# Kernel optimization log

Hardware: AMD Instinct MI355X
Metric: run time of the kernel (lower is better)

## Reference

```python
import jax, jax.numpy as jnp
import numpy as np

N, C, A = 4096, 1000, 2048


def setup_inputs() -> dict:
    key = jax.random.key(0)
    k1, k2, k3, k4 = jax.random.split(key, 4)
    features = jax.random.normal(k1, (N, A), dtype=jnp.float32)
    labels = jax.random.randint(k2, (N,), 0, C, dtype=jnp.int64)
    cv_matrix = jax.random.uniform(k3, (N, A), dtype=jnp.float32)
    ratio = jnp.asarray(0.5, dtype=jnp.float32)
    weight = jax.random.normal(k4, (C, A), dtype=jnp.float32) * 0.02
    bias = jnp.zeros((C,), dtype=jnp.float32)
    return {"features": features, "labels": labels, "cv_matrix": cv_matrix,
            "ratio": ratio, "weight": weight, "bias": bias}


def reference(features, labels, cv_matrix, ratio, weight, bias):
    # logits = features @ W^T + b
    logits = features @ weight.T + bias  # [N, C]
    # sigma2[n,c] = ratio * sum_a (W[c,a] - W[y_n,a])^2 * cv[n,a]
    # Expand the square to avoid materializing the [N, C, A] tensor:
    #   = sum_a W[c,a]^2 cv - 2 sum_a W[c,a] (W[y,a] cv) + sum_a W[y,a]^2 cv
    Wy = weight[labels]                          # [N, A] gather of per-label rows
    t1 = cv_matrix @ (weight * weight).T         # [N, C]
    t2 = (cv_matrix * Wy) @ weight.T             # [N, C]
    t3 = jnp.sum(Wy * Wy * cv_matrix, axis=1, keepdims=True)  # [N, 1]
    sigma2 = ratio * (t1 - 2.0 * t2 + t3)        # [N, C]
    aug_logits = logits + 0.5 * sigma2
    # mean cross-entropy on augmented logits
    logp = jax.nn.log_softmax(aug_logits, axis=-1)
    nll = -jnp.take_along_axis(logp, labels[:, None], axis=1)[:, 0]
    loss = jnp.mean(nll)
    return loss, logits
```

## Files before the change

kernel.cpp:

```cpp
#include <hip/hip_runtime.h>
#include <hip/hip_bf16.h>

#define N_ROWS 4096
#define C_CLS  1000
#define C_PAD  1024
#define A_DIM  2048

typedef __attribute__((ext_vector_type(8))) short short8;
typedef __attribute__((ext_vector_type(4))) float f32x4;

__device__ __forceinline__ unsigned short f2bf(float x) {
    unsigned u = __float_as_uint(x);
    unsigned rounding = 0x7fffu + ((u >> 16) & 1u);
    return (unsigned short)((u + rounding) >> 16);
}

__device__ __forceinline__ unsigned pack2(float a, float b) {
    return (unsigned)f2bf(a) | ((unsigned)f2bf(b) << 16);
}

__device__ __forceinline__ void gload16(unsigned short* lds, const unsigned short* g) {
    __builtin_amdgcn_global_load_lds(
        (const __attribute__((address_space(1))) unsigned int*)g,
        (__attribute__((address_space(3))) unsigned int*)lds,
        16, 0, 0);
}

__global__ __launch_bounds__(256) void prep_all(
        const float* __restrict__ F, const float* __restrict__ CV,
        const float* __restrict__ W, const int* __restrict__ labels,
        const float* __restrict__ ratio_p,
        unsigned short* __restrict__ Fb, unsigned short* __restrict__ Ub,
        unsigned short* __restrict__ Vb,
        unsigned short* __restrict__ Wb, unsigned short* __restrict__ W2b,
        float* __restrict__ t3c) {
    int bid = blockIdx.x;
    if (bid >= N_ROWS) {
        int t = (bid - N_ROWS) * 256 + threadIdx.x;
        int a8 = t * 8;
        int c = a8 >> 11;
        int a = a8 & (A_DIM - 1);
        float4 w0 = make_float4(0.f, 0.f, 0.f, 0.f);
        float4 w1 = make_float4(0.f, 0.f, 0.f, 0.f);
        if (c < C_CLS) {
            w0 = *(const float4*)(W + (size_t)c * A_DIM + a);
            w1 = *(const float4*)(W + (size_t)c * A_DIM + a + 4);
        }
        uint4 pw, pw2;
        pw.x  = pack2(w0.x, w0.y);  pw.y  = pack2(w0.z, w0.w);
        pw.z  = pack2(w1.x, w1.y);  pw.w  = pack2(w1.z, w1.w);
        pw2.x = pack2(w0.x*w0.x, w0.y*w0.y);  pw2.y = pack2(w0.z*w0.z, w0.w*w0.w);
        pw2.z = pack2(w1.x*w1.x, w1.y*w1.y);  pw2.w = pack2(w1.z*w1.z, w1.w*w1.w);
        *(uint4*)(Wb  + (size_t)a8) = pw;
        *(uint4*)(W2b + (size_t)a8) = pw2;
        return;
    }
    int n = bid;
    int y = labels[n];
    float ratio = ratio_p[0];
    float hr = 0.5f * ratio;
    const float* frow  = F  + (size_t)n * A_DIM;
    const float* cvrow = CV + (size_t)n * A_DIM;
    const float* wyrow = W  + (size_t)y * A_DIM;
    size_t obase = (size_t)n * A_DIM;

    int a = threadIdx.x * 8;
    float4 f0  = *(const float4*)(frow + a);
    float4 f1  = *(const float4*)(frow + a + 4);
    float4 c0  = *(const float4*)(cvrow + a);
    float4 c1  = *(const float4*)(cvrow + a + 4);
    float4 y0  = *(const float4*)(wyrow + a);
    float4 y1  = *(const float4*)(wyrow + a + 4);

    float s = y0.x*y0.x*c0.x + y0.y*y0.y*c0.y + y0.z*y0.z*c0.z + y0.w*y0.w*c0.w
            + y1.x*y1.x*c1.x + y1.y*y1.y*c1.y + y1.z*y1.z*c1.z + y1.w*y1.w*c1.w;

    uint4 pf, pu, pv;
    pf.x = pack2(f0.x, f0.y);  pf.y = pack2(f0.z, f0.w);
    pf.z = pack2(f1.x, f1.y);  pf.w = pack2(f1.z, f1.w);
    pu.x = pack2(f0.x - ratio*c0.x*y0.x, f0.y - ratio*c0.y*y0.y);
    pu.y = pack2(f0.z - ratio*c0.z*y0.z, f0.w - ratio*c0.w*y0.w);
    pu.z = pack2(f1.x - ratio*c1.x*y1.x, f1.y - ratio*c1.y*y1.y);
    pu.w = pack2(f1.z - ratio*c1.z*y1.z, f1.w - ratio*c1.w*y1.w);
    pv.x = pack2(hr*c0.x, hr*c0.y);  pv.y = pack2(hr*c0.z, hr*c0.w);
    pv.z = pack2(hr*c1.x, hr*c1.y);  pv.w = pack2(hr*c1.z, hr*c1.w);
    *(uint4*)(Fb + obase + a) = pf;
    *(uint4*)(Ub + obase + a) = pu;
    *(uint4*)(Vb + obase + a) = pv;

    for (int off = 32; off; off >>= 1) s += __shfl_down(s, off);
    __shared__ float wsum[4];
    int lane = threadIdx.x & 63, wid = threadIdx.x >> 6;
    if (lane == 0) wsum[wid] = s;
    __syncthreads();
    if (threadIdx.x == 0)
        t3c[n] = hr * (wsum[0] + wsum[1] + wsum[2] + wsum[3]);
}

#define BM 128
#define BN 128
#define BK 32
#define TILE_USH (BM * BK)
#define BUF_USH  (5 * TILE_USH)
#define NT       (A_DIM / BK)

__global__ __launch_bounds__(256, 1) void gemm_fused(
        const unsigned short* __restrict__ Fb, const unsigned short* __restrict__ Ub,
        const unsigned short* __restrict__ Vb, const unsigned short* __restrict__ Wb,
        const unsigned short* __restrict__ W2b,
        const float* __restrict__ t3c, const float* __restrict__ bias,
        float* __restrict__ out_logits, float* __restrict__ aug) {
    __shared__ unsigned short lds[2 * BUF_USH];

    int bid = blockIdx.x;
    int bn = bid & 7;
    int bm = bid >> 3;

    int tid = threadIdx.x;
    int lane = tid & 63, wid = tid >> 6;
    int wm = wid >> 1, wn = wid & 1;

    int srow = lane >> 2;
    int scs  = ((lane & 3) * 8) ^ (((srow >> 1) & 3) << 3);
    int r0 = wid * 16 + srow;
    size_t gA0 = (size_t)(bm * BM + r0) * A_DIM + scs;
    size_t gB0 = (size_t)(bn * BN + r0) * A_DIM + scs;
    const size_t gStep = (size_t)64 * A_DIM;
    int d0 = wid * 512;
    int d1 = 2048 + wid * 512;

    int fr = lane & 15;
    int kof = ((lane >> 4) * 8) ^ (((fr >> 1) & 3) << 3);
    int aoff = fr * BK + kof;

    f32x4 accL[4][4] = {};
    f32x4 accA[4][4] = {};

    {
        unsigned short* b = lds;
        gload16(b + 0*TILE_USH + d0, Fb  + gA0);
        gload16(b + 0*TILE_USH + d1, Fb  + gA0 + gStep);
        gload16(b + 1*TILE_USH + d0, Ub  + gA0);
        gload16(b + 1*TILE_USH + d1, Ub  + gA0 + gStep);
        gload16(b + 2*TILE_USH + d0, Vb  + gA0);
        gload16(b + 2*TILE_USH + d1, Vb  + gA0 + gStep);
        gload16(b + 3*TILE_USH + d0, Wb  + gB0);
        gload16(b + 3*TILE_USH + d1, Wb  + gB0 + gStep);
        gload16(b + 4*TILE_USH + d0, W2b + gB0);
        gload16(b + 4*TILE_USH + d1, W2b + gB0 + gStep);
    }
    __syncthreads();

    for (int t = 0; t < NT; t++) {
        unsigned short* cbuf = lds + (t & 1) * BUF_USH;
        if (t + 1 < NT) {
            unsigned short* b = lds + ((t + 1) & 1) * BUF_USH;
            size_t ka = gA0 + (size_t)(t + 1) * BK;
            size_t kb = gB0 + (size_t)(t + 1) * BK;
            gload16(b + 0*TILE_USH + d0, Fb  + ka);
            gload16(b + 0*TILE_USH + d1, Fb  + ka + gStep);
            gload16(b + 1*TILE_USH + d0, Ub  + ka);
            gload16(b + 1*TILE_USH + d1, Ub  + ka + gStep);
            gload16(b + 2*TILE_USH + d0, Vb  + ka);
            gload16(b + 2*TILE_USH + d1, Vb  + ka + gStep);
            gload16(b + 3*TILE_USH + d0, Wb  + kb);
            gload16(b + 3*TILE_USH + d1, Wb  + kb + gStep);
            gload16(b + 4*TILE_USH + d0, W2b + kb);
            gload16(b + 4*TILE_USH + d1, W2b + kb + gStep);
        }

        short8 aF[4], aU[4], aV[4], bWf[4], bW2f[4];
        #pragma unroll
        for (int m = 0; m < 4; m++) {
            int off = wm * 2048 + m * 512 + aoff;
            aF[m] = *(const short8*)(cbuf + 0*TILE_USH + off);
            aU[m] = *(const short8*)(cbuf + 1*TILE_USH + off);
            aV[m] = *(const short8*)(cbuf + 2*TILE_USH + off);
        }
        #pragma unroll
        for (int n = 0; n < 4; n++) {
            int off = wn * 2048 + n * 512 + aoff;
            bWf[n]  = *(const short8*)(cbuf + 3*TILE_USH + off);
            bW2f[n] = *(const short8*)(cbuf + 4*TILE_USH + off);
        }
        #pragma unroll
        for (int m = 0; m < 4; m++)
            #pragma unroll
            for (int n = 0; n < 4; n++) {
                accL[m][n] = __builtin_amdgcn_mfma_f32_16x16x32_bf16(aF[m], bWf[n],  accL[m][n], 0, 0, 0);
                accA[m][n] = __builtin_amdgcn_mfma_f32_16x16x32_bf16(aU[m], bWf[n],  accA[m][n], 0, 0, 0);
                accA[m][n] = __builtin_amdgcn_mfma_f32_16x16x32_bf16(aV[m], bW2f[n], accA[m][n], 0, 0, 0);
            }

        __syncthreads();
    }

    #pragma unroll
    for (int n = 0; n < 4; n++) {
        int col = bn * BN + wn * 64 + n * 16 + fr;
        if (col < C_CLS) {
            float bv = bias[col];
            #pragma unroll
            for (int m = 0; m < 4; m++) {
                int rbase = bm * BM + wm * 64 + m * 16 + (lane >> 4) * 4;
                #pragma unroll
                for (int j = 0; j < 4; j++) {
                    int row = rbase + j;
                    out_logits[(size_t)row * C_CLS + col] = accL[m][n][j] + bv;
                    aug[(size_t)row * C_PAD + col] = accA[m][n][j] + bv + t3c[row];
                }
            }
        }
    }
}

__global__ __launch_bounds__(256) void softmax_nll(const float* __restrict__ aug,
                                                   const int* __restrict__ labels,
                                                   float* __restrict__ nll) {
    int n = blockIdx.x;
    const float* row = aug + (size_t)n * C_PAD;
    int lane = threadIdx.x & 63, wid = threadIdx.x >> 6;
    __shared__ float sm[4], ss[4];

    float mx = -1e30f;
    for (int c = threadIdx.x; c < C_CLS; c += 256) mx = fmaxf(mx, row[c]);
    for (int off = 32; off; off >>= 1) mx = fmaxf(mx, __shfl_down(mx, off));
    if (lane == 0) sm[wid] = mx;
    __syncthreads();
    mx = fmaxf(fmaxf(sm[0], sm[1]), fmaxf(sm[2], sm[3]));

    float s = 0.f;
    for (int c = threadIdx.x; c < C_CLS; c += 256) s += __expf(row[c] - mx);
    for (int off = 32; off; off >>= 1) s += __shfl_down(s, off);
    if (lane == 0) ss[wid] = s;
    __syncthreads();
    if (threadIdx.x == 0) {
        float tot = ss[0] + ss[1] + ss[2] + ss[3];
        nll[n] = logf(tot) + mx - row[labels[n]];
    }
}

__global__ __launch_bounds__(256) void final_reduce(const float* __restrict__ nll,
                                                    float* __restrict__ out_loss) {
    float s = 0.f;
    for (int i = threadIdx.x; i < N_ROWS; i += 256) s += nll[i];
    for (int off = 32; off; off >>= 1) s += __shfl_down(s, off);
    __shared__ float ss[4];
    int lane = threadIdx.x & 63, wid = threadIdx.x >> 6;
    if (lane == 0) ss[wid] = s;
    __syncthreads();
    if (threadIdx.x == 0)
        out_loss[0] = (ss[0] + ss[1] + ss[2] + ss[3]) / (float)N_ROWS;
}

extern "C" void kernel_launch(void* const* d_in, const int* in_sizes, int n_in,
                              void* d_out, int out_size, void* d_ws, size_t ws_size,
                              hipStream_t stream) {
    const float* features = (const float*)d_in[0];
    const int*   labels   = (const int*)d_in[1];
    const float* cv       = (const float*)d_in[2];
    const float* ratio    = (const float*)d_in[3];
    const float* weight   = (const float*)d_in[4];
    const float* bias     = (const float*)d_in[5];
    float* out = (float*)d_out;

    char* p = (char*)d_ws;
    unsigned short* Wb  = (unsigned short*)p; p += (size_t)C_PAD * A_DIM * 2;
    unsigned short* W2b = (unsigned short*)p; p += (size_t)C_PAD * A_DIM * 2;
    unsigned short* Fb  = (unsigned short*)p; p += (size_t)N_ROWS * A_DIM * 2;
    unsigned short* Ub  = (unsigned short*)p; p += (size_t)N_ROWS * A_DIM * 2;
    unsigned short* Vb  = (unsigned short*)p; p += (size_t)N_ROWS * A_DIM * 2;
    float* t3c = (float*)p; p += (size_t)N_ROWS * 4;
    float* aug = (float*)p; p += (size_t)N_ROWS * C_PAD * 4;
    float* nllb = (float*)p; p += (size_t)N_ROWS * 4;

    int wprep_blocks = (C_PAD * A_DIM / 8) / 256;
    prep_all<<<N_ROWS + wprep_blocks, 256, 0, stream>>>(
        features, cv, weight, labels, ratio, Fb, Ub, Vb, Wb, W2b, t3c);
    gemm_fused<<<(N_ROWS / BM) * (C_PAD / BN), 256, 0, stream>>>(
        Fb, Ub, Vb, Wb, W2b, t3c, bias, out + 1, aug);
    softmax_nll<<<N_ROWS, 256, 0, stream>>>(aug, labels, nllb);
    final_reduce<<<1, 256, 0, stream>>>(nllb, out);
}
```

Measured before the change: 243.4 us.

## Halve GEMM N-tile with XCD-aware mapping, store augmented logits in bf16

Narrows the fused GEMM's N tile from 128 to 64, which doubles the block count. It allows two blocks per CU and remaps block ids so each XCD handles a pair of N tiles for better L2 reuse of the weight tiles. The augmented logits intermediate is now stored as bf16, halving its write and read traffic, and the softmax kernel reads one 8-element vector per thread. The trade-off is that A-side operand tiles are reloaded for twice as many blocks, and the bf16 logits lower loss precision.

```diff
diff --git a/kernel.cpp b/kernel.cpp
--- a/kernel.cpp
+++ b/kernel.cpp
@@ -13,6 +13,10 @@
     unsigned u = __float_as_uint(x);
     unsigned rounding = 0x7fffu + ((u >> 16) & 1u);
     return (unsigned short)((u + rounding) >> 16);
+}
+
+__device__ __forceinline__ float bf2f(unsigned short u) {
+    return __uint_as_float((unsigned)u << 16);
 }
 
 __device__ __forceinline__ unsigned pack2(float a, float b) {
@@ -98,23 +102,25 @@
 }
 
 #define BM 128
-#define BN 128
+#define BN 64
 #define BK 32
-#define TILE_USH (BM * BK)
-#define BUF_USH  (5 * TILE_USH)
-#define NT       (A_DIM / BK)
-
-__global__ __launch_bounds__(256, 1) void gemm_fused(
+#define TILE_A (BM * BK)
+#define TILE_B (BN * BK)
+#define BUF_USH (3 * TILE_A + 2 * TILE_B)
+#define NT (A_DIM / BK)
+
+__global__ __launch_bounds__(256, 2) void gemm_fused(
         const unsigned short* __restrict__ Fb, const unsigned short* __restrict__ Ub,
         const unsigned short* __restrict__ Vb, const unsigned short* __restrict__ Wb,
         const unsigned short* __restrict__ W2b,
         const float* __restrict__ t3c, const float* __restrict__ bias,
-        float* __restrict__ out_logits, float* __restrict__ aug) {
+        float* __restrict__ out_logits, unsigned short* __restrict__ aug) {
     __shared__ unsigned short lds[2 * BUF_USH];
 
     int bid = blockIdx.x;
-    int bn = bid & 7;
-    int bm = bid >> 3;
+    int xcd = bid & 7, idx = bid >> 3;
+    int bn = (xcd << 1) | (idx & 1);
+    int bm = idx >> 1;
 
     int tid = threadIdx.x;
     int lane = tid & 63, wid = tid >> 6;
@@ -133,21 +139,19 @@
     int kof = ((lane >> 4) * 8) ^ (((fr >> 1) & 3) << 3);
     int aoff = fr * BK + kof;
 
-    f32x4 accL[4][4] = {};
-    f32x4 accA[4][4] = {};
+    f32x4 accL[4][2] = {};
+    f32x4 accA[4][2] = {};
 
     {
         unsigned short* b = lds;
-        gload16(b + 0*TILE_USH + d0, Fb  + gA0);
-        gload16(b + 0*TILE_USH + d1, Fb  + gA0 + gStep);
-        gload16(b + 1*TILE_USH + d0, Ub  + gA0);
-        gload16(b + 1*TILE_USH + d1, Ub  + gA0 + gStep);
-        gload16(b + 2*TILE_USH + d0, Vb  + gA0);
-        gload16(b + 2*TILE_USH + d1, Vb  + gA0 + gStep);
-        gload16(b + 3*TILE_USH + d0, Wb  + gB0);
-        gload16(b + 3*TILE_USH + d1, Wb  + gB0 + gStep);
-        gload16(b + 4*TILE_USH + d0, W2b + gB0);
-        gload16(b + 4*TILE_USH + d1, W2b + gB0 + gStep);
+        gload16(b + 0*TILE_A + d0, Fb + gA0);
+        gload16(b + 0*TILE_A + d1, Fb + gA0 + gStep);
+        gload16(b + 1*TILE_A + d0, Ub + gA0);
+        gload16(b + 1*TILE_A + d1, Ub + gA0 + gStep);
+        gload16(b + 2*TILE_A + d0, Vb + gA0);
+        gload16(b + 2*TILE_A + d1, Vb + gA0 + gStep);
+        gload16(b + 3*TILE_A + d0,          Wb  + gB0);
+        gload16(b + 3*TILE_A + TILE_B + d0, W2b + gB0);
     }
     __syncthreads();
 
@@ -157,36 +161,34 @@
             unsigned short* b = lds + ((t + 1) & 1) * BUF_USH;
             size_t ka = gA0 + (size_t)(t + 1) * BK;
             size_t kb = gB0 + (size_t)(t + 1) * BK;
-            gload16(b + 0*TILE_USH + d0, Fb  + ka);
-            gload16(b + 0*TILE_USH + d1, Fb  + ka + gStep);
-            gload16(b + 1*TILE_USH + d0, Ub  + ka);
-            gload16(b + 1*TILE_USH + d1, Ub  + ka + gStep);
-            gload16(b + 2*TILE_USH + d0, Vb  + ka);
-            gload16(b + 2*TILE_USH + d1, Vb  + ka + gStep);
-            gload16(b + 3*TILE_USH + d0, Wb  + kb);
-            gload16(b + 3*TILE_USH + d1, Wb  + kb + gStep);
-            gload16(b + 4*TILE_USH + d0, W2b + kb);
-            gload16(b + 4*TILE_USH + d1, W2b + kb + gStep);
-        }
-
-        short8 aF[4], aU[4], aV[4], bWf[4], bW2f[4];
+            gload16(b + 0*TILE_A + d0, Fb + ka);
+            gload16(b + 0*TILE_A + d1, Fb + ka + gStep);
+            gload16(b + 1*TILE_A + d0, Ub + ka);
+            gload16(b + 1*TILE_A + d1, Ub + ka + gStep);
+            gload16(b + 2*TILE_A + d0, Vb + ka);
+            gload16(b + 2*TILE_A + d1, Vb + ka + gStep);
+            gload16(b + 3*TILE_A + d0,          Wb  + kb);
+            gload16(b + 3*TILE_A + TILE_B + d0, W2b + kb);
+        }
+
+        short8 aF[4], aU[4], aV[4], bWf[2], bW2f[2];
         #pragma unroll
         for (int m = 0; m < 4; m++) {
             int off = wm * 2048 + m * 512 + aoff;
-            aF[m] = *(const short8*)(cbuf + 0*TILE_USH + off);
-            aU[m] = *(const short8*)(cbuf + 1*TILE_USH + off);
-            aV[m] = *(const short8*)(cbuf + 2*TILE_USH + off);
-        }
-        #pragma unroll
-        for (int n = 0; n < 4; n++) {
-            int off = wn * 2048 + n * 512 + aoff;
-            bWf[n]  = *(const short8*)(cbuf + 3*TILE_USH + off);
-            bW2f[n] = *(const short8*)(cbuf + 4*TILE_USH + off);
+            aF[m] = *(const short8*)(cbuf + 0*TILE_A + off);
+            aU[m] = *(const short8*)(cbuf + 1*TILE_A + off);
+            aV[m] = *(const short8*)(cbuf + 2*TILE_A + off);
+        }
+        #pragma unroll
+        for (int n = 0; n < 2; n++) {
+            int off = wn * 1024 + n * 512 + aoff;
+            bWf[n]  = *(const short8*)(cbuf + 3*TILE_A + off);
+            bW2f[n] = *(const short8*)(cbuf + 3*TILE_A + TILE_B + off);
         }
         #pragma unroll
         for (int m = 0; m < 4; m++)
             #pragma unroll
-            for (int n = 0; n < 4; n++) {
+            for (int n = 0; n < 2; n++) {
                 accL[m][n] = __builtin_amdgcn_mfma_f32_16x16x32_bf16(aF[m], bWf[n],  accL[m][n], 0, 0, 0);
                 accA[m][n] = __builtin_amdgcn_mfma_f32_16x16x32_bf16(aU[m], bWf[n],  accA[m][n], 0, 0, 0);
                 accA[m][n] = __builtin_amdgcn_mfma_f32_16x16x32_bf16(aV[m], bW2f[n], accA[m][n], 0, 0, 0);
@@ -196,8 +198,8 @@
     }
 
     #pragma unroll
-    for (int n = 0; n < 4; n++) {
-        int col = bn * BN + wn * 64 + n * 16 + fr;
+    for (int n = 0; n < 2; n++) {
+        int col = bn * BN + wn * 32 + n * 16 + fr;
         if (col < C_CLS) {
             float bv = bias[col];
             #pragma unroll
@@ -207,36 +209,49 @@
                 for (int j = 0; j < 4; j++) {
                     int row = rbase + j;
                     out_logits[(size_t)row * C_CLS + col] = accL[m][n][j] + bv;
-                    aug[(size_t)row * C_PAD + col] = accA[m][n][j] + bv + t3c[row];
+                    aug[(size_t)row * C_PAD + col] = f2bf(accA[m][n][j] + bv + t3c[row]);
                 }
             }
         }
     }
 }
 
-__global__ __launch_bounds__(256) void softmax_nll(const float* __restrict__ aug,
+__global__ __launch_bounds__(256) void softmax_nll(const unsigned short* __restrict__ aug,
                                                    const int* __restrict__ labels,
                                                    float* __restrict__ nll) {
     int n = blockIdx.x;
-    const float* row = aug + (size_t)n * C_PAD;
-    int lane = threadIdx.x & 63, wid = threadIdx.x >> 6;
+    const unsigned short* row = aug + (size_t)n * C_PAD;
+    int tid = threadIdx.x;
+    int lane = tid & 63, wid = tid >> 6;
     __shared__ float sm[4], ss[4];
 
+    float v[8];
+    bool act = tid < (C_CLS / 8);
     float mx = -1e30f;
-    for (int c = threadIdx.x; c < C_CLS; c += 256) mx = fmaxf(mx, row[c]);
+    if (act) {
+        short8 r8 = *(const short8*)(row + tid * 8);
+        #pragma unroll
+        for (int j = 0; j < 8; j++) {
+            v[j] = bf2f((unsigned short)r8[j]);
+            mx = fmaxf(mx, v[j]);
+        }
+    }
     for (int off = 32; off; off >>= 1) mx = fmaxf(mx, __shfl_down(mx, off));
     if (lane == 0) sm[wid] = mx;
     __syncthreads();
     mx = fmaxf(fmaxf(sm[0], sm[1]), fmaxf(sm[2], sm[3]));
 
     float s = 0.f;
-    for (int c = threadIdx.x; c < C_CLS; c += 256) s += __expf(row[c] - mx);
+    if (act) {
+        #pragma unroll
+        for (int j = 0; j < 8; j++) s += __expf(v[j] - mx);
+    }
     for (int off = 32; off; off >>= 1) s += __shfl_down(s, off);
     if (lane == 0) ss[wid] = s;
     __syncthreads();
-    if (threadIdx.x == 0) {
+    if (tid == 0) {
         float tot = ss[0] + ss[1] + ss[2] + ss[3];
-        nll[n] = logf(tot) + mx - row[labels[n]];
+        nll[n] = logf(tot) + mx - bf2f(row[labels[n]]);
     }
 }
 
@@ -271,7 +286,7 @@
     unsigned short* Ub  = (unsigned short*)p; p += (size_t)N_ROWS * A_DIM * 2;
     unsigned short* Vb  = (unsigned short*)p; p += (size_t)N_ROWS * A_DIM * 2;
     float* t3c = (float*)p; p += (size_t)N_ROWS * 4;
-    float* aug = (float*)p; p += (size_t)N_ROWS * C_PAD * 4;
+    unsigned short* aug = (unsigned short*)p; p += (size_t)N_ROWS * C_PAD * 2;
     float* nllb = (float*)p; p += (size_t)N_ROWS * 4;
 
     int wprep_blocks = (C_PAD * A_DIM / 8) / 256;
```

After: 214.8 us. 11.8% less time.
